# Performance work log

Hardware: AMD Instinct MI355X
Metric: run time of the kernel (lower is better)

Reference implementation:

```python
import jax, jax.numpy as jnp
import numpy as np

N_NODES = 50000
N_EDGES = 400000
D = 128


def _rgg_layer(x, src, tgt, Wk, Wq, Wv, Ws, b, n_nodes):
    # Node-level projections (dense GEMMs, as in PyG which applies Linear before message passing)
    k = x @ Wk  # lin_key, gathered at targets
    q = x @ Wq  # lin_query, gathered at sources
    v = x @ Wv  # lin_value, gathered at sources
    # Per-edge gather + sigmoid gate + elementwise message
    eta = jax.nn.sigmoid(k[tgt] + q[src])  # [E, D]
    msg = eta * v[src]                      # [E, D]
    # Scatter-add aggregation to target nodes
    agg = jax.ops.segment_sum(msg, tgt, num_segments=n_nodes)
    # Root/skip connection + bias
    return agg + x @ Ws + b


def setup_inputs() -> dict:
    key = jax.random.key(0)
    ks = jax.random.split(key, 12)
    s = 1.0 / np.sqrt(D)
    x = jax.random.normal(ks[0], (N_NODES, D), dtype=jnp.float32)
    edge_index = jax.random.randint(ks[1], (2, N_EDGES), 0, N_NODES, dtype=jnp.int64)
    W = lambda k: (jax.random.normal(k, (D, D), dtype=jnp.float32) * s)
    return {
        "x": x,
        "edge_index": edge_index,
        "Wk1": W(ks[2]), "Wq1": W(ks[3]), "Wv1": W(ks[4]), "Ws1": W(ks[5]),
        "b1": jnp.zeros((D,), dtype=jnp.float32),
        "Wk2": W(ks[6]), "Wq2": W(ks[7]), "Wv2": W(ks[8]), "Ws2": W(ks[9]),
        "b2": jnp.zeros((D,), dtype=jnp.float32),
    }


def reference(x, edge_index, Wk1, Wq1, Wv1, Ws1, b1, Wk2, Wq2, Wv2, Ws2, b2):
    src, tgt = edge_index[0], edge_index[1]
    n = x.shape[0]
    h = _rgg_layer(x, src, tgt, Wk1, Wq1, Wv1, Ws1, b1, n)
    h = jax.nn.relu(h)
    # F.dropout treated as identity (deterministic/inference reference)
    out = _rgg_layer(h, src, tgt, Wk2, Wq2, Wv2, Ws2, b2, n)
    return out
```

## Files before the change

kernel.cpp:

```cpp
#include <hip/hip_runtime.h>

#define N_NODES 50000
#define D 128
#define N_EDGES 400000
#define NCHUNKS ((N_NODES + 255) / 256)
#define NBLK64 ((N_NODES + 63) / 64)
#define W_FRAG_SHORTS 16384

typedef short s8v  __attribute__((ext_vector_type(8)));
typedef float f4v  __attribute__((ext_vector_type(4)));

__device__ __forceinline__ unsigned int f2bf(float f) {
    unsigned int u = __float_as_uint(f);
    u += 0x7FFFu + ((u >> 16) & 1u);
    return u >> 16;
}
__device__ __forceinline__ unsigned int packbf(float a, float b) {
    return (f2bf(b) << 16) | f2bf(a);
}
__device__ __forceinline__ float bflo(unsigned int u) { return __uint_as_float(u << 16); }
__device__ __forceinline__ float bfhi(unsigned int u) { return __uint_as_float(u & 0xFFFF0000u); }
__device__ __forceinline__ float sigm(float x) {
    return __builtin_amdgcn_rcpf(1.f + __expf(-x));
}

__global__ __launch_bounds__(256)
void cvt_bf16(const float* __restrict__ X, short* __restrict__ Xb)
{
    const size_t i = ((size_t)blockIdx.x * 256 + threadIdx.x) * 8;
    float4 a0 = *(const float4*)(X + i);
    float4 a1 = *(const float4*)(X + i + 4);
    s8v v;
    v[0] = (short)f2bf(a0.x); v[1] = (short)f2bf(a0.y);
    v[2] = (short)f2bf(a0.z); v[3] = (short)f2bf(a0.w);
    v[4] = (short)f2bf(a1.x); v[5] = (short)f2bf(a1.y);
    v[6] = (short)f2bf(a1.z); v[7] = (short)f2bf(a1.w);
    *(s8v*)(Xb + i) = v;
}

__global__ __launch_bounds__(256)
void make_wt(const float* __restrict__ W0, const float* __restrict__ W1,
             const float* __restrict__ W2, const float* __restrict__ W3,
             const float* __restrict__ W4, const float* __restrict__ W5,
             const float* __restrict__ W6, const float* __restrict__ W7,
             short* __restrict__ Wt)
{
    const int wsel = blockIdx.x;
    const float* W = (wsel == 0) ? W0 : (wsel == 1) ? W1 : (wsel == 2) ? W2 :
                     (wsel == 3) ? W3 : (wsel == 4) ? W4 : (wsel == 5) ? W5 :
                     (wsel == 6) ? W6 : W7;
    const int slot = blockIdx.y * 256 + threadIdx.x;
    const int frag = slot >> 6;
    const int lane = slot & 63;
    const int n    = (frag >> 2) * 16 + (lane & 15);
    const int kc   = frag & 3;
    const int quad = lane >> 4;
    const int k0   = kc * 32 + quad * 8;

    s8v v;
#pragma unroll
    for (int j = 0; j < 8; ++j)
        v[j] = (short)f2bf(W[(size_t)(k0 + j) * D + n]);
    *(s8v*)(Wt + (size_t)wsel * W_FRAG_SHORTS + (size_t)slot * 8) = v;
}

__global__ __launch_bounds__(256)
void gemm_all(const short* __restrict__ Xb, const short* __restrict__ WtL,
              const float* __restrict__ bias,
              short* __restrict__ Kb, unsigned int* __restrict__ QV,
              float* __restrict__ Agg)
{
    __shared__ __align__(16) short As[8192];
    __shared__ __align__(16) short Bs[16384];
    __shared__ __align__(16) float biasS[128];

    const int tid  = threadIdx.x;
    const int lane = tid & 63;
    const int w    = tid >> 6;
    const int wr   = w & 1;
    const int wc   = w >> 1;
    const int m0   = blockIdx.x * 64;

    if (tid < 128) biasS[tid] = bias[tid];

#pragma unroll
    for (int i = 0; i < 4; ++i) {
        const int m   = (tid >> 4) + 16 * i;
        const int oct = tid & 15;
        const int row = m0 + m;
        s8v v = (s8v){0, 0, 0, 0, 0, 0, 0, 0};
        if (row < N_NODES) v = *(const s8v*)(Xb + (size_t)row * D + oct * 8);
        const int kc = oct >> 2, quad = oct & 3;
        const int frag = (m >> 4) * 4 + kc;
        const int slot = ((m & 15) + 16 * quad) ^ (kc << 1);
        *(s8v*)&As[frag * 512 + slot * 8] = v;
    }

    float* Cs = (float*)Bs;

    for (int sel = 0; sel < 4; ++sel) {
        __syncthreads();

        const short* Wf = WtL + (size_t)sel * W_FRAG_SHORTS;
#pragma unroll
        for (int j = 0; j < 8; ++j) {
            const int chunk = tid + 256 * j;
            __builtin_amdgcn_global_load_lds(
                (const __attribute__((address_space(1))) unsigned int*)(Wf + chunk * 8),
                (__attribute__((address_space(3))) unsigned int*)(&Bs[(chunk & ~63) * 8]),
                16, 0, 0);
        }
        __syncthreads();

        f4v acc[2][4];
#pragma unroll
        for (int mt = 0; mt < 2; ++mt)
#pragma unroll
            for (int nt = 0; nt < 4; ++nt)
                acc[mt][nt] = (f4v){0.f, 0.f, 0.f, 0.f};

#pragma unroll
        for (int kc = 0; kc < 4; ++kc) {
            const int sl = (lane ^ (kc << 1)) * 8;
            s8v a0 = *(const s8v*)&As[((2 * wr + 0) * 4 + kc) * 512 + sl];
            s8v a1 = *(const s8v*)&As[((2 * wr + 1) * 4 + kc) * 512 + sl];
#pragma unroll
            for (int nt = 0; nt < 4; ++nt) {
                s8v b = *(const s8v*)&Bs[((4 * wc + nt) * 4 + kc) * 512 + lane * 8];
                acc[0][nt] = __builtin_amdgcn_mfma_f32_16x16x32_bf16(a0, b, acc[0][nt], 0, 0, 0);
                acc[1][nt] = __builtin_amdgcn_mfma_f32_16x16x32_bf16(a1, b, acc[1][nt], 0, 0, 0);
            }
        }
        __syncthreads();

#pragma unroll
        for (int mt = 0; mt < 2; ++mt) {
            const int r0 = wr * 32 + mt * 16 + (lane >> 4) * 4;
#pragma unroll
            for (int nt = 0; nt < 4; ++nt) {
                const int col = wc * 64 + nt * 16 + (lane & 15);
                const int g = col >> 2, jj = col & 3;
#pragma unroll
                for (int i = 0; i < 4; ++i) {
                    const int row = r0 + i;
                    const int gs  = g ^ (((row >> 2) & 3) << 2);
                    Cs[row * 128 + gs * 4 + jj] = acc[mt][nt][i];
                }
            }
        }
        __syncthreads();

#pragma unroll
        for (int j = 0; j < 8; ++j) {
            const int c    = tid + 256 * j;
            const int row  = c >> 5;
            const int gg   = c & 31;
            const int gs   = gg ^ (((row >> 2) & 3) << 2);
            const f4v vv   = *(const f4v*)&Cs[row * 128 + gs * 4];
            const int grow = m0 + row;
            if (grow >= N_NODES) continue;
            if (sel == 3) {
                const float4 bv = *(const float4*)&biasS[gg * 4];
                float4 o = make_float4(vv[0] + bv.x, vv[1] + bv.y,
                                       vv[2] + bv.z, vv[3] + bv.w);
                *(float4*)&Agg[(size_t)grow * D + gg * 4] = o;
            } else {
                const unsigned int p0 = packbf(vv[0], vv[1]);
                const unsigned int p1 = packbf(vv[2], vv[3]);
                if (sel == 0) {
                    uint2* kp = (uint2*)((unsigned int*)Kb + (size_t)grow * 64 + gg * 2);
                    *kp = make_uint2(p0, p1);
                } else {
                    unsigned int* rowp = QV + (size_t)grow * 128 + gg * 4 + (sel == 2 ? 1 : 0);
                    rowp[0] = p0; rowp[2] = p1;
                }
            }
        }
    }
}

__global__ __launch_bounds__(256)
void hist_kernel(const int* __restrict__ tgt, int* __restrict__ counts)
{
    int e = blockIdx.x * 256 + threadIdx.x;
    if (e < N_EDGES) atomicAdd(&counts[tgt[e]], 1);
}

__global__ __launch_bounds__(256)
void chunk_reduce(const int* __restrict__ counts, int* __restrict__ chunk_sum)
{
    __shared__ int s[256];
    int i = blockIdx.x * 256 + threadIdx.x;
    s[threadIdx.x] = (i < N_NODES) ? counts[i] : 0;
    __syncthreads();
    for (int d = 128; d > 0; d >>= 1) {
        if (threadIdx.x < d) s[threadIdx.x] += s[threadIdx.x + d];
        __syncthreads();
    }
    if (threadIdx.x == 0) chunk_sum[blockIdx.x] = s[0];
}

__global__ void scan_sums(const int* __restrict__ chunk_sum,
                          int* __restrict__ chunk_off, int* __restrict__ off)
{
    if (threadIdx.x == 0) {
        int run = 0;
        for (int i = 0; i < NCHUNKS; ++i) { chunk_off[i] = run; run += chunk_sum[i]; }
        off[N_NODES] = run;
    }
}

__global__ __launch_bounds__(256)
void scan_chunks(const int* __restrict__ counts, const int* __restrict__ chunk_off,
                 int* __restrict__ off, int* __restrict__ cursor)
{
    __shared__ int s[256];
    int i = blockIdx.x * 256 + threadIdx.x;
    int v = (i < N_NODES) ? counts[i] : 0;
    s[threadIdx.x] = v;
    __syncthreads();
    for (int d = 1; d < 256; d <<= 1) {
        int t = (threadIdx.x >= d) ? s[threadIdx.x - d] : 0;
        __syncthreads();
        s[threadIdx.x] += t;
        __syncthreads();
    }
    if (i < N_NODES) {
        int excl = s[threadIdx.x] - v + chunk_off[blockIdx.x];
        off[i]    = excl;
        cursor[i] = excl;
    }
}

__global__ __launch_bounds__(256)
void scatter_kernel(const int* __restrict__ src, const int* __restrict__ tgt,
                    int* __restrict__ cursor, int* __restrict__ es)
{
    int e = blockIdx.x * 256 + threadIdx.x;
    if (e < N_EDGES) {
        int pos = atomicAdd(&cursor[tgt[e]], 1);
        es[pos] = src[e];
    }
}

template<bool FIRST>
__global__ __launch_bounds__(256)
void node_agg(const int* __restrict__ off, const int* __restrict__ es,
              const short* __restrict__ K, const unsigned int* __restrict__ QV,
              const float* __restrict__ Skip, float* __restrict__ OutF,
              unsigned int* __restrict__ Hb)
{
    const int lane = threadIdx.x & 63;
    const int t    = __builtin_amdgcn_readfirstlane(blockIdx.x * 4 + (threadIdx.x >> 6));

    const unsigned int ku = ((const unsigned int*)K)[(size_t)t * 64 + lane];
    const float kx = bflo(ku), ky = bfhi(ku);

    float ax = 0.f, ay = 0.f, bx = 0.f, by = 0.f;
    const int e0 = __builtin_amdgcn_readfirstlane(off[t]);
    const int e1 = __builtin_amdgcn_readfirstlane(off[t + 1]);

    int e = e0;
    for (; e + 2 <= e1; e += 2) {
        const int s0 = __builtin_amdgcn_readfirstlane(es[e]);
        const int s1 = __builtin_amdgcn_readfirstlane(es[e + 1]);
        const uint2 qv0 = ((const uint2*)(QV + (size_t)s0 * 128))[lane];
        const uint2 qv1 = ((const uint2*)(QV + (size_t)s1 * 128))[lane];
        ax += bflo(qv0.y) * sigm(kx + bflo(qv0.x));
        ay += bfhi(qv0.y) * sigm(ky + bfhi(qv0.x));
        bx += bflo(qv1.y) * sigm(kx + bflo(qv1.x));
        by += bfhi(qv1.y) * sigm(ky + bfhi(qv1.x));
    }
    if (e < e1) {
        const int s0 = __builtin_amdgcn_readfirstlane(es[e]);
        const uint2 qv0 = ((const uint2*)(QV + (size_t)s0 * 128))[lane];
        ax += bflo(qv0.y) * sigm(kx + bflo(qv0.x));
        ay += bfhi(qv0.y) * sigm(ky + bfhi(qv0.x));
    }

    const float2 sk = ((const float2*)Skip)[(size_t)t * 64 + lane];
    const float rx = sk.x + ax + bx;
    const float ry = sk.y + ay + by;

    if (FIRST) {
        Hb[(size_t)t * 64 + lane] = packbf(fmaxf(rx, 0.f), fmaxf(ry, 0.f));
    } else {
        ((float2*)OutF)[(size_t)t * 64 + lane] = make_float2(rx, ry);
    }
}

extern "C" void kernel_launch(void* const* d_in, const int* in_sizes, int n_in,
                              void* d_out, int out_size, void* d_ws, size_t ws_size,
                              hipStream_t stream)
{
    const float* x   = (const float*)d_in[0];
    const int*   ei  = (const int*)d_in[1];
    const float* Wk1 = (const float*)d_in[2];
    const float* Wq1 = (const float*)d_in[3];
    const float* Wv1 = (const float*)d_in[4];
    const float* Ws1 = (const float*)d_in[5];
    const float* b1  = (const float*)d_in[6];
    const float* Wk2 = (const float*)d_in[7];
    const float* Wq2 = (const float*)d_in[8];
    const float* Wv2 = (const float*)d_in[9];
    const float* Ws2 = (const float*)d_in[10];
    const float* b2  = (const float*)d_in[11];

    const int* src = ei;
    const int* tgt = ei + N_EDGES;

    const size_t nd = (size_t)N_NODES * D;
    short* kb  = (short*)d_ws;
    short* qv  = kb + nd;
    short* xb  = qv + 2 * nd;
    short* hb  = xb + nd;
    float* agg1 = (float*)(hb + nd);
    short* wt  = (short*)(agg1 + nd);
    int* counts    = (int*)(wt + 8 * W_FRAG_SHORTS);
    int* off       = counts + N_NODES;
    int* cursor    = off + N_NODES + 1;
    int* es        = cursor + N_NODES;
    int* chunk_sum = es + N_EDGES;
    int* chunk_off = chunk_sum + NCHUNKS;
    float* out = (float*)d_out;

    const int eb = (N_EDGES + 255) / 256;

    cvt_bf16<<<(int)(nd / (256 * 8)), 256, 0, stream>>>(x, xb);
    make_wt<<<dim3(8, 8), 256, 0, stream>>>(Wk1, Wq1, Wv1, Ws1, Wk2, Wq2, Wv2, Ws2, wt);
    hipMemsetAsync(counts, 0, N_NODES * sizeof(int), stream);
    hist_kernel   <<<eb, 256, 0, stream>>>(tgt, counts);
    chunk_reduce  <<<NCHUNKS, 256, 0, stream>>>(counts, chunk_sum);
    scan_sums     <<<1, 64, 0, stream>>>(chunk_sum, chunk_off, off);
    scan_chunks   <<<NCHUNKS, 256, 0, stream>>>(counts, chunk_off, off, cursor);
    scatter_kernel<<<eb, 256, 0, stream>>>(src, tgt, cursor, es);

    gemm_all<<<NBLK64, 256, 0, stream>>>(xb, wt, b1, kb, (unsigned int*)qv, agg1);
    node_agg<true><<<N_NODES / 4, 256, 0, stream>>>(off, es, kb, (const unsigned int*)qv,
                                                    agg1, nullptr, (unsigned int*)hb);

    gemm_all<<<NBLK64, 256, 0, stream>>>(hb, wt + 4 * W_FRAG_SHORTS, b2,
                                         kb, (unsigned int*)qv, out);
    node_agg<false><<<N_NODES / 4, 256, 0, stream>>>(off, es, kb, (const unsigned int*)qv,
                                                     out, out, nullptr);
}
```

Before: 275.6 us.

## Merge prep kernels, parallelize chunk scan, unroll edge gather by four

```diff
diff --git a/kernel.cpp b/kernel.cpp
--- a/kernel.cpp
+++ b/kernel.cpp
@@ -7,6 +7,11 @@
 #define NBLK64 ((N_NODES + 63) / 64)
 #define W_FRAG_SHORTS 16384
 
+#define CVT_BLOCKS 3125
+#define MW_BLOCKS  64
+#define HIST_BLOCKS ((N_EDGES + 255) / 256)
+#define PREP_BLOCKS (CVT_BLOCKS + MW_BLOCKS + HIST_BLOCKS)
+
 typedef short s8v  __attribute__((ext_vector_type(8)));
 typedef float f4v  __attribute__((ext_vector_type(4)));
 
@@ -25,43 +30,47 @@
 }
 
 __global__ __launch_bounds__(256)
-void cvt_bf16(const float* __restrict__ X, short* __restrict__ Xb)
-{
-    const size_t i = ((size_t)blockIdx.x * 256 + threadIdx.x) * 8;
-    float4 a0 = *(const float4*)(X + i);
-    float4 a1 = *(const float4*)(X + i + 4);
-    s8v v;
-    v[0] = (short)f2bf(a0.x); v[1] = (short)f2bf(a0.y);
-    v[2] = (short)f2bf(a0.z); v[3] = (short)f2bf(a0.w);
-    v[4] = (short)f2bf(a1.x); v[5] = (short)f2bf(a1.y);
-    v[6] = (short)f2bf(a1.z); v[7] = (short)f2bf(a1.w);
-    *(s8v*)(Xb + i) = v;
-}
-
-__global__ __launch_bounds__(256)
-void make_wt(const float* __restrict__ W0, const float* __restrict__ W1,
-             const float* __restrict__ W2, const float* __restrict__ W3,
-             const float* __restrict__ W4, const float* __restrict__ W5,
-             const float* __restrict__ W6, const float* __restrict__ W7,
-             short* __restrict__ Wt)
-{
-    const int wsel = blockIdx.x;
-    const float* W = (wsel == 0) ? W0 : (wsel == 1) ? W1 : (wsel == 2) ? W2 :
-                     (wsel == 3) ? W3 : (wsel == 4) ? W4 : (wsel == 5) ? W5 :
-                     (wsel == 6) ? W6 : W7;
-    const int slot = blockIdx.y * 256 + threadIdx.x;
-    const int frag = slot >> 6;
-    const int lane = slot & 63;
-    const int n    = (frag >> 2) * 16 + (lane & 15);
-    const int kc   = frag & 3;
-    const int quad = lane >> 4;
-    const int k0   = kc * 32 + quad * 8;
-
-    s8v v;
-#pragma unroll
-    for (int j = 0; j < 8; ++j)
-        v[j] = (short)f2bf(W[(size_t)(k0 + j) * D + n]);
-    *(s8v*)(Wt + (size_t)wsel * W_FRAG_SHORTS + (size_t)slot * 8) = v;
+void prep_all(const float* __restrict__ X, short* __restrict__ Xb,
+              const float* __restrict__ W0, const float* __restrict__ W1,
+              const float* __restrict__ W2, const float* __restrict__ W3,
+              const float* __restrict__ W4, const float* __restrict__ W5,
+              const float* __restrict__ W6, const float* __restrict__ W7,
+              short* __restrict__ Wt,
+              const int* __restrict__ tgt, int* __restrict__ counts)
+{
+    const int b = blockIdx.x;
+    if (b < CVT_BLOCKS) {
+        const size_t i = ((size_t)b * 256 + threadIdx.x) * 8;
+        float4 a0 = *(const float4*)(X + i);
+        float4 a1 = *(const float4*)(X + i + 4);
+        s8v v;
+        v[0] = (short)f2bf(a0.x); v[1] = (short)f2bf(a0.y);
+        v[2] = (short)f2bf(a0.z); v[3] = (short)f2bf(a0.w);
+        v[4] = (short)f2bf(a1.x); v[5] = (short)f2bf(a1.y);
+        v[6] = (short)f2bf(a1.z); v[7] = (short)f2bf(a1.w);
+        *(s8v*)(Xb + i) = v;
+    } else if (b < CVT_BLOCKS + MW_BLOCKS) {
+        const int bb   = b - CVT_BLOCKS;
+        const int wsel = bb >> 3;
+        const float* W = (wsel == 0) ? W0 : (wsel == 1) ? W1 : (wsel == 2) ? W2 :
+                         (wsel == 3) ? W3 : (wsel == 4) ? W4 : (wsel == 5) ? W5 :
+                         (wsel == 6) ? W6 : W7;
+        const int slot = (bb & 7) * 256 + threadIdx.x;
+        const int frag = slot >> 6;
+        const int lane = slot & 63;
+        const int n    = (frag >> 2) * 16 + (lane & 15);
+        const int kc   = frag & 3;
+        const int quad = lane >> 4;
+        const int k0   = kc * 32 + quad * 8;
+        s8v v;
+#pragma unroll
+        for (int j = 0; j < 8; ++j)
+            v[j] = (short)f2bf(W[(size_t)(k0 + j) * D + n]);
+        *(s8v*)(Wt + (size_t)wsel * W_FRAG_SHORTS + (size_t)slot * 8) = v;
+    } else {
+        const int e = (b - CVT_BLOCKS - MW_BLOCKS) * 256 + threadIdx.x;
+        if (e < N_EDGES) atomicAdd(&counts[tgt[e]], 1);
+    }
 }
 
 __global__ __launch_bounds__(256)
@@ -180,13 +189,6 @@
 }
 
 __global__ __launch_bounds__(256)
-void hist_kernel(const int* __restrict__ tgt, int* __restrict__ counts)
-{
-    int e = blockIdx.x * 256 + threadIdx.x;
-    if (e < N_EDGES) atomicAdd(&counts[tgt[e]], 1);
-}
-
-__global__ __launch_bounds__(256)
 void chunk_reduce(const int* __restrict__ counts, int* __restrict__ chunk_sum)
 {
     __shared__ int s[256];
@@ -200,14 +202,23 @@
     if (threadIdx.x == 0) chunk_sum[blockIdx.x] = s[0];
 }
 
-__global__ void scan_sums(const int* __restrict__ chunk_sum,
-                          int* __restrict__ chunk_off, int* __restrict__ off)
-{
-    if (threadIdx.x == 0) {
-        int run = 0;
-        for (int i = 0; i < NCHUNKS; ++i) { chunk_off[i] = run; run += chunk_sum[i]; }
-        off[N_NODES] = run;
-    }
+__global__ __launch_bounds__(256)
+void scan_sums(const int* __restrict__ chunk_sum,
+               int* __restrict__ chunk_off, int* __restrict__ off)
+{
+    __shared__ int s[256];
+    const int tid = threadIdx.x;
+    const int v = (tid < NCHUNKS) ? chunk_sum[tid] : 0;
+    s[tid] = v;
+    __syncthreads();
+    for (int d = 1; d < 256; d <<= 1) {
+        int t = (tid >= d) ? s[tid - d] : 0;
+        __syncthreads();
+        s[tid] += t;
+        __syncthreads();
+    }
+    if (tid < NCHUNKS) chunk_off[tid] = s[tid] - v;
+    if (tid == NCHUNKS - 1) off[N_NODES] = s[tid];
 }
 
 __global__ __launch_bounds__(256)
@@ -255,32 +266,41 @@
 
     const unsigned int ku = ((const unsigned int*)K)[(size_t)t * 64 + lane];
     const float kx = bflo(ku), ky = bfhi(ku);
+    const float2 sk = ((const float2*)Skip)[(size_t)t * 64 + lane];
 
     float ax = 0.f, ay = 0.f, bx = 0.f, by = 0.f;
+    float cx = 0.f, cy = 0.f, dx = 0.f, dy = 0.f;
     const int e0 = __builtin_amdgcn_readfirstlane(off[t]);
     const int e1 = __builtin_amdgcn_readfirstlane(off[t + 1]);
 
     int e = e0;
-    for (; e + 2 <= e1; e += 2) {
+    for (; e + 4 <= e1; e += 4) {
         const int s0 = __builtin_amdgcn_readfirstlane(es[e]);
         const int s1 = __builtin_amdgcn_readfirstlane(es[e + 1]);
+        const int s2 = __builtin_amdgcn_readfirstlane(es[e + 2]);
+        const int s3 = __builtin_amdgcn_readfirstlane(es[e + 3]);
         const uint2 qv0 = ((const uint2*)(QV + (size_t)s0 * 128))[lane];
         const uint2 qv1 = ((const uint2*)(QV + (size_t)s1 * 128))[lane];
+        const uint2 qv2 = ((const uint2*)(QV + (size_t)s2 * 128))[lane];
+        const uint2 qv3 = ((const uint2*)(QV + (size_t)s3 * 128))[lane];
         ax += bflo(qv0.y) * sigm(kx + bflo(qv0.x));
         ay += bfhi(qv0.y) * sigm(ky + bfhi(qv0.x));
         bx += bflo(qv1.y) * sigm(kx + bflo(qv1.x));
         by += bfhi(qv1.y) * sigm(ky + bfhi(qv1.x));
-    }
-    if (e < e1) {
+        cx += bflo(qv2.y) * sigm(kx + bflo(qv2.x));
+        cy += bfhi(qv2.y) * sigm(ky + bfhi(qv2.x));
+        dx += bflo(qv3.y) * sigm(kx + bflo(qv3.x));
+        dy += bfhi(qv3.y) * sigm(ky + bfhi(qv3.x));
+    }
+    for (; e < e1; ++e) {
         const int s0 = __builtin_amdgcn_readfirstlane(es[e]);
         const uint2 qv0 = ((const uint2*)(QV + (size_t)s0 * 128))[lane];
         ax += bflo(qv0.y) * sigm(kx + bflo(qv0.x));
         ay += bfhi(qv0.y) * sigm(ky + bfhi(qv0.x));
     }
 
-    const float2 sk = ((const float2*)Skip)[(size_t)t * 64 + lane];
-    const float rx = sk.x + ax + bx;
-    const float ry = sk.y + ay + by;
+    const float rx = sk.x + (ax + bx) + (cx + dx);
+    const float ry = sk.y + (ay + by) + (cy + dy);
 
     if (FIRST) {
         Hb[(size_t)t * 64 + lane] = packbf(fmaxf(rx, 0.f), fmaxf(ry, 0.f));
@@ -324,16 +344,14 @@
     int* chunk_off = chunk_sum + NCHUNKS;
     float* out = (float*)d_out;
 
-    const int eb = (N_EDGES + 255) / 256;
-
-    cvt_bf16<<<(int)(nd / (256 * 8)), 256, 0, stream>>>(x, xb);
-    make_wt<<<dim3(8, 8), 256, 0, stream>>>(Wk1, Wq1, Wv1, Ws1, Wk2, Wq2, Wv2, Ws2, wt);
     hipMemsetAsync(counts, 0, N_NODES * sizeof(int), stream);
-    hist_kernel   <<<eb, 256, 0, stream>>>(tgt, counts);
+    prep_all<<<PREP_BLOCKS, 256, 0, stream>>>(x, xb,
+                                              Wk1, Wq1, Wv1, Ws1, Wk2, Wq2, Wv2, Ws2,
+                                              wt, tgt, counts);
     chunk_reduce  <<<NCHUNKS, 256, 0, stream>>>(counts, chunk_sum);
-    scan_sums     <<<1, 64, 0, stream>>>(chunk_sum, chunk_off, off);
+    scan_sums     <<<1, 256, 0, stream>>>(chunk_sum, chunk_off, off);
     scan_chunks   <<<NCHUNKS, 256, 0, stream>>>(counts, chunk_off, off, cursor);
-    scatter_kernel<<<eb, 256, 0, stream>>>(src, tgt, cursor, es);
+    scatter_kernel<<<HIST_BLOCKS, 256, 0, stream>>>(src, tgt, cursor, es);
 
     gemm_all<<<NBLK64, 256, 0, stream>>>(xb, wt, b1, kb, (unsigned int*)qv, agg1);
     node_agg<true><<<N_NODES / 4, 256, 0, stream>>>(off, es, kb, (const unsigned int*)qv,
```

Measured after the change: 268.7 us. 2.5% less time.
